# Kernel optimization log

Measured on AMD Instinct MI355X. Metric: run time of the kernel, lower is better.

## Reference

```python
import jax, jax.numpy as jnp
import numpy as np
from jax import lax

STATE_LEN = 5
N_BASE = 4
N_STATES = N_BASE ** STATE_LEN      # 1024
ALPHA_LEN = N_BASE + 1              # 5 (blank + 4 bases)
BLANK_SCORE = 2.0
SCALE = 5.0
NEG = -1e30                         # log-zero surrogate (avoids -inf NaNs)

def _make_idx():
    s = np.arange(N_STATES)
    stay = s[:, None]
    # torch: arange(1024).repeat_interleave(4).reshape(4,-1).T -> idx[j,1+b] = b*256 + j//4
    move = np.repeat(s, N_BASE).reshape(N_BASE, -1).T
    return jnp.asarray(np.concatenate([stay, move], axis=1), dtype=jnp.int32)  # (1024,5)

IDX = _make_idx()

def _logZ_full(scores):
    # full-lattice logZ; scores (T,N,5120)
    T, N, C = scores.shape
    Ms = scores.reshape(T, N, N_STATES, ALPHA_LEN)
    def step(alpha, Mt):
        a = alpha[:, IDX]                          # (N,1024,5) gather of predecessors
        return jax.nn.logsumexp(a + Mt, axis=-1), None
    alpha0 = jnp.zeros((N, N_STATES), scores.dtype)
    alphaT, _ = lax.scan(step, alpha0, Ms)
    return jax.nn.logsumexp(alphaT, axis=-1)       # (N,)

def _prepare_ctc_scores(scores, targets):
    # scores (T,N,C), targets (N,Lmax) base ids in 1..4
    t = jnp.clip(targets - 1, 0)
    T, N, C = scores.shape
    Lmax = t.shape[1]
    n = Lmax - (STATE_LEN - 1)
    stay_idx = sum(t[:, i:n + i] * (N_BASE ** (STATE_LEN - i - 1)) for i in range(STATE_LEN)) * ALPHA_LEN
    move_idx = stay_idx[:, 1:] + t[:, :n - 1] + 1
    stay = jnp.take_along_axis(scores, jnp.broadcast_to(stay_idx[None], (T, N, n)), axis=2)
    move = jnp.take_along_axis(scores, jnp.broadcast_to(move_idx[None], (T, N, n - 1)), axis=2)
    return stay, move

def _ctc_logZ(stay, move, lens):
    # stay (T,N,L), move (T,N,L-1), lens (N,) effective kmer-path lengths
    T, N, L = stay.shape
    alpha0 = jnp.full((N, L), NEG, stay.dtype).at[:, 0].set(0.0)
    def step(alpha, sm):
        s, m = sm
        moved = jnp.pad(alpha[:, :-1] + m, ((0, 0), (1, 0)), constant_values=NEG)
        return jnp.logaddexp(alpha + s, moved), None
    alphaT, _ = lax.scan(step, alpha0, (stay, move))
    return alphaT[jnp.arange(N), lens - 1]

def setup_inputs() -> dict:
    key = jax.random.key(0)
    k1, k2, k3, k4, k5, k6 = jax.random.split(key, 6)
    B, T, D, Lmax = 16, 512, 512, 256
    hs_pad = jax.random.normal(k1, (B, T, D), dtype=jnp.float32)
    hlens = jnp.full((B,), T, dtype=jnp.int32)
    ys_pad = jax.random.randint(k2, (B, Lmax), 1, 5, dtype=jnp.int32)
    ys_lens = jax.random.randint(k3, (B,), 64, Lmax + 1, dtype=jnp.int32)
    W = jax.random.normal(k4, (4096, D), dtype=jnp.float32) * 0.02
    b = jax.random.normal(k5, (4096,), dtype=jnp.float32) * 0.01
    return {"hs_pad": hs_pad, "hlens": hlens, "ys_pad": ys_pad, "ys_lens": ys_lens, "W": W, "b": b}

def reference(hs_pad, hlens, ys_pad, ys_lens, W, b):
    x = jnp.transpose(hs_pad, (1, 0, 2))                 # (T,B,D)
    scores = jnp.tanh(x @ W.T + b) * SCALE               # (T,N,4096)
    T, N, C = scores.shape
    scores = jnp.pad(scores.reshape(T, N, C // N_BASE, N_BASE),
                     ((0, 0), (0, 0), (0, 0), (1, 0)), constant_values=BLANK_SCORE)
    scores = scores.reshape(T, N, -1).astype(jnp.float32)  # (T,N,5120)
    # normalise: subtract full-lattice logZ / T
    logZ = _logZ_full(scores)
    norm = scores - logZ[:, None] / T                    # (N,1) broadcasts over (T,N,C)
    stay, move = _prepare_ctc_scores(norm, ys_pad)
    logz = _ctc_logZ(stay, move, ys_lens + 1 - STATE_LEN)
    loss = -(logz / ys_lens.astype(scores.dtype))        # (N,) (reduction=None in forward)
    scores_bt = jnp.transpose(scores, (1, 0, 2))
    return loss, scores_bt, scores_bt
```

## Files before the change

### kernel.cpp

```cpp
#include <hip/hip_runtime.h>
#include <hip/hip_bf16.h>
#include <hip/hip_fp16.h>
#include <math.h>

#define T_STEPS 512
#define NB      16
#define D_IN    512
#define CG      4096
#define CO      5120
#define LMAX    252
#define NEGF    (-1e30f)
#define SCORES_SZ 41943040LL
#define L2E 1.4426950408889634f
#define LN2 0.6931471805599453f
#define STAYT 0.36787944117144233f

typedef __attribute__((ext_vector_type(8))) short bf16x8;
typedef __attribute__((ext_vector_type(4))) float f32x4;

__device__ __forceinline__ float tanh5(float x) {
    x = fminf(fmaxf(x, -15.f), 15.f);
    float e = __expf(2.f * x);
    return 5.f * (e - 1.f) / (e + 1.f);
}
__device__ __forceinline__ unsigned short f2bf(float v) {
    __hip_bfloat16 h = __float2bfloat16(v);
    return *reinterpret_cast<unsigned short*>(&h);
}
__device__ __forceinline__ float h2f(unsigned short s) {
    union { unsigned short u; _Float16 h; } c; c.u = s;
    return (float)c.h;
}
__device__ __forceinline__ unsigned short f2h(float v) {
    union { unsigned short u; _Float16 h; } c; c.h = (_Float16)v;
    return c.u;
}
__device__ __forceinline__ void cvt8(uint4 u, float* g) {
    g[0] = h2f((unsigned short)(u.x & 0xffff)); g[1] = h2f((unsigned short)(u.x >> 16));
    g[2] = h2f((unsigned short)(u.y & 0xffff)); g[3] = h2f((unsigned short)(u.y >> 16));
    g[4] = h2f((unsigned short)(u.z & 0xffff)); g[5] = h2f((unsigned short)(u.z >> 16));
    g[6] = h2f((unsigned short)(u.w & 0xffff)); g[7] = h2f((unsigned short)(u.w >> 16));
}
__device__ __forceinline__ void xbar() {
    __builtin_amdgcn_sched_barrier(0);
    asm volatile("s_waitcnt lgkmcnt(0)");
    __builtin_amdgcn_s_barrier();
    __builtin_amdgcn_sched_barrier(0);
}
__device__ __forceinline__ void gll16(const unsigned short* g, unsigned short* l) {
    __builtin_amdgcn_global_load_lds((const __attribute__((address_space(1))) void*)g,
                                     (__attribute__((address_space(3))) void*)l, 16, 0, 0);
}

__global__ __launch_bounds__(256) void cvt_bf16_kernel(const float* __restrict__ src,
                                                       unsigned short* __restrict__ dst,
                                                       int n4) {
    int i = blockIdx.x * 256 + threadIdx.x;
    if (i < n4) {
        float4 v = *(reinterpret_cast<const float4*>(src) + i);
        ushort4 o;
        o.x = f2bf(v.x); o.y = f2bf(v.y); o.z = f2bf(v.z); o.w = f2bf(v.w);
        *(reinterpret_cast<ushort4*>(dst) + i) = o;
    }
}

template <bool WSE>
__global__ __launch_bounds__(256) void crf_gemm_bf16(
    const unsigned short* __restrict__ A16,
    const unsigned short* __restrict__ W16,
    const float* __restrict__ bias,
    float* __restrict__ out,
    unsigned short* __restrict__ e16)
{
    __shared__ unsigned short As[128 * 64];
    __shared__ unsigned short Bs[128 * 64];
    const int tid  = threadIdx.x;
    const int lane = tid & 63;
    const int wv   = __builtin_amdgcn_readfirstlane(tid >> 6);
    const int wr   = wv >> 1, wc = wv & 1;
    const int m0   = blockIdx.y * 128;
    const int n0   = blockIdx.x * 128;
    const int wbase = tid & 192;

    f32x4 acc[4][4];
    #pragma unroll
    for (int i = 0; i < 4; ++i)
        #pragma unroll
        for (int j = 0; j < 4; ++j) acc[i][j] = (f32x4){0.f, 0.f, 0.f, 0.f};

    const int l15 = lane & 15, lj = lane >> 4, l7 = lane & 7;

    for (int k0 = 0; k0 < D_IN; k0 += 64) {
        __syncthreads();
        #pragma unroll
        for (int i = 0; i < 4; ++i) {
            const int c   = i * 256 + tid;
            const int row = c >> 3;
            const int jg  = (c & 7) ^ (row & 7);
            const unsigned short* ga = A16 + (size_t)(m0 + row) * D_IN + k0 + jg * 8;
            const unsigned short* gb = W16 + (size_t)(n0 + row) * D_IN + k0 + jg * 8;
            gll16(ga, As + (size_t)(i * 256 + wbase) * 8);
            gll16(gb, Bs + (size_t)(i * 256 + wbase) * 8);
        }
        __syncthreads();
        #pragma unroll
        for (int ks = 0; ks < 2; ++ks) {
            bf16x8 af[4], bb[4];
            #pragma unroll
            for (int mi = 0; mi < 4; ++mi) {
                const int row = wr * 64 + mi * 16 + l15;
                const int jsw = (ks * 4 + lj) ^ l7;
                af[mi] = *reinterpret_cast<const bf16x8*>(&As[row * 64 + jsw * 8]);
            }
            #pragma unroll
            for (int ni = 0; ni < 4; ++ni) {
                const int row = wc * 64 + ni * 16 + l15;
                const int jsw = (ks * 4 + lj) ^ l7;
                bb[ni] = *reinterpret_cast<const bf16x8*>(&Bs[row * 64 + jsw * 8]);
            }
            #pragma unroll
            for (int mi = 0; mi < 4; ++mi)
                #pragma unroll
                for (int ni = 0; ni < 4; ++ni)
                    acc[mi][ni] = __builtin_amdgcn_mfma_f32_16x16x32_bf16(
                        af[mi], bb[ni], acc[mi][ni], 0, 0, 0);
        }
    }

    float bv[4];
    #pragma unroll
    for (int ni = 0; ni < 4; ++ni) bv[ni] = bias[n0 + wc * 64 + ni * 16 + l15];

    #pragma unroll
    for (int mi = 0; mi < 4; ++mi) {
        #pragma unroll
        for (int r = 0; r < 4; ++r) {
            const int m = m0 + wr * 64 + mi * 16 + lj * 4 + r;
            float* r1 = out + 16 + (size_t)m * CO;
            #pragma unroll
            for (int ni = 0; ni < 4; ++ni) {
                const int n = n0 + wc * 64 + ni * 16 + l15;
                const float v = tanh5(acc[mi][ni][r] + bv[ni]);
                const int ch = (n >> 2) * 5 + (n & 3) + 1;
                r1[ch] = v;
                r1[ch + SCORES_SZ] = v;
                if ((l15 & 3) == 0) {
                    r1[ch - 1] = 2.0f;
                    r1[ch - 1 + SCORES_SZ] = 2.0f;
                }
                if (WSE) e16[(size_t)m * CG + n] = f2h(__expf(v - 3.0f));
            }
        }
    }
}

__global__ __launch_bounds__(256) void fb2_kernel(
    const unsigned short* __restrict__ e16,
    const int* __restrict__ ys_pad,
    const int* __restrict__ ys_lens,
    float* __restrict__ FA, float* __restrict__ FAe,
    float* __restrict__ FB, float* __restrict__ FBe,
    float* __restrict__ CAL, float* __restrict__ CBE)
{
    __shared__ float buf[2][1024];
    __shared__ float wmax4[4];
    __shared__ int tcl[256];
    const int role = blockIdx.x >> 4;
    const int n = blockIdx.x & 15;
    const int q = threadIdx.x;
    const int w = q >> 6, lane = q & 63;
    if (role < 2) {
        const bool FWD = (role == 0);
        const unsigned short* eb = e16 + (size_t)(n * T_STEPS) * CG + 16 * q;
        float P0 = 1.f, P1 = 1.f, P2 = 1.f, P3 = 1.f, acc = 0.f;
        *(float4*)&buf[0][4 * q] = make_float4(1.f, 1.f, 1.f, 1.f);
        uint4 pf[8][2];
        #pragma unroll
        for (int u = 0; u < 8; ++u) {
            const int row = FWD ? u : (511 - u);
            pf[u][0] = *(const uint4*)(eb + (size_t)row * CG);
            pf[u][1] = *(const uint4*)(eb + (size_t)row * CG + 8);
        }
        xbar();
        int cur = 0;
        for (int t = 0; t < 256; t += 8) {
            #pragma unroll
            for (int u = 0; u < 8; ++u) {
                float g[16];
                cvt8(pf[u][0], g);
                cvt8(pf[u][1], g + 8);
                int tn = t + u + 8; if (tn > 255) tn = 255;
                const int row = FWD ? tn : (511 - tn);
                pf[u][0] = *(const uint4*)(eb + (size_t)row * CG);
                pf[u][1] = *(const uint4*)(eb + (size_t)row * CG + 8);
                float n0, n1, n2, n3;
                if (FWD) {
                    const float b0 = buf[cur][q];
                    const float b1 = buf[cur][q + 256];
                    const float b2 = buf[cur][q + 512];
                    const float b3 = buf[cur][q + 768];
                    n0 = fmaf(STAYT, P0, fmaf(g[0],  b0, g[1]  * b1) + fmaf(g[2],  b2, g[3]  * b3));
                    n1 = fmaf(STAYT, P1, fmaf(g[4],  b0, g[5]  * b1) + fmaf(g[6],  b2, g[7]  * b3));
                    n2 = fmaf(STAYT, P2, fmaf(g[8],  b0, g[9]  * b1) + fmaf(g[10], b2, g[11] * b3));
                    n3 = fmaf(STAYT, P3, fmaf(g[12], b0, g[13] * b1) + fmaf(g[14], b2, g[15] * b3));
                } else {
                    const float4 b4 = *(const float4*)&buf[cur][4 * q];
                    n0 = fmaf(STAYT, P0, fmaf(g[0], b4.x, g[4] * b4.y) + fmaf(g[8],  b4.z, g[12] * b4.w));
                    n1 = fmaf(STAYT, P1, fmaf(g[1], b4.x, g[5] * b4.y) + fmaf(g[9],  b4.z, g[13] * b4.w));
                    n2 = fmaf(STAYT, P2, fmaf(g[2], b4.x, g[6] * b4.y) + fmaf(g[10], b4.z, g[14] * b4.w));
                    n3 = fmaf(STAYT, P3, fmaf(g[3], b4.x, g[7] * b4.y) + fmaf(g[11], b4.z, g[15] * b4.w));
                }
                if (((t + u) & 7) == 1) {
                    const float wm = fmaxf(fmaxf(wmax4[0], wmax4[1]), fmaxf(wmax4[2], wmax4[3]));
                    const int e = (int)((__float_as_uint(wm) >> 23) & 0xff) - 127;
                    const float c = __uint_as_float((unsigned)(127 - e) << 23);
                    n0 *= c; n1 *= c; n2 *= c; n3 *= c;
                    acc += (float)e;
                }
                P0 = n0; P1 = n1; P2 = n2; P3 = n3;
                if (FWD) {
                    *(float4*)&buf[cur ^ 1][4 * q] = make_float4(P0, P1, P2, P3);
                } else {
                    buf[cur ^ 1][q]       = P0;
                    buf[cur ^ 1][q + 256] = P1;
                    buf[cur ^ 1][q + 512] = P2;
                    buf[cur ^ 1][q + 768] = P3;
                }
                if (((t + u) & 7) == 0) {
                    float m = fmaxf(fmaxf(P0, P1), fmaxf(P2, P3));
                    #pragma unroll
                    for (int msk = 1; msk < 64; msk <<= 1)
                        m = fmaxf(m, __shfl_xor(m, msk, 64));
                    if (lane == 0) wmax4[w] = m;
                }
                xbar();
                cur ^= 1;
            }
        }
        if (FWD) {
            *(float4*)&FA[n * 1024 + 4 * q] = make_float4(P0, P1, P2, P3);
            if (q == 0) FAe[n] = acc;
        } else {
            FB[n * 1024 + q]       = P0;
            FB[n * 1024 + q + 256] = P1;
            FB[n * 1024 + q + 512] = P2;
            FB[n * 1024 + q + 768] = P3;
            if (q == 0) FBe[n] = acc;
        }
    } else {
        float* abuf = &buf[0][0];
        const bool FWD = (role == 2);
        tcl[q] = max(ys_pad[n * 256 + q] - 1, 0);
        xbar();
        int mch = 0; bool val;
        if (FWD) {
            val = (q >= 1 && q < LMAX);
            if (val) {
                const int code = tcl[q] * 256 + tcl[q + 1] * 64 + tcl[q + 2] * 16
                               + tcl[q + 3] * 4 + tcl[q + 4];
                mch = code * 4 + tcl[q - 1];
            }
        } else {
            val = (q < LMAX - 1);
            if (val) {
                const int code = tcl[q + 1] * 256 + tcl[q + 2] * 64 + tcl[q + 3] * 16
                               + tcl[q + 4] * 4 + tcl[q + 5];
                mch = code * 4 + tcl[q];
            }
        }
        const int li = ys_lens[n] - 5;
        float a = FWD ? ((q == 0) ? 0.f : NEGF)
                      : ((q == li) ? 0.f : NEGF);
        abuf[q] = a;
        const unsigned short* eb = e16 + (size_t)(n * T_STEPS) * CG + mch;
        unsigned short pv[16];
        #pragma unroll
        for (int s = 0; s < 16; ++s) {
            const int row = FWD ? s : (511 - s);
            pv[s] = eb[(size_t)row * CG];
        }
        xbar();
        const float STAY2 = (2.0f - 3.0f) * L2E;
        int cur = 0;
        for (int t = 0; t < 256; t += 16) {
            #pragma unroll
            for (int u = 0; u < 16; ++u) {
                const float g2 = val ? __builtin_amdgcn_logf(h2f(pv[u])) : NEGF;
                int tn = t + u + 16; if (tn > 255) tn = 255;
                const int row = FWD ? tn : (511 - tn);
                pv[u] = eb[(size_t)row * CG];
                float nb;
                if (FWD) nb = (q > 0)   ? abuf[cur * 256 + q - 1] : NEGF;
                else     nb = (q < 255) ? abuf[cur * 256 + q + 1] : NEGF;
                const float st = a + STAY2;
                const float mv = nb + g2;
                const float mx = fmaxf(st, mv);
                const float mn = fminf(st, mv);
                a = mx + __builtin_amdgcn_logf(1.f + __builtin_amdgcn_exp2f(mn - mx));
                abuf[(cur ^ 1) * 256 + q] = a;
                xbar();
                cur ^= 1;
            }
        }
        if (FWD) CAL[n * 256 + q] = a;
        else     CBE[n * 256 + q] = a;
    }
}

__global__ __launch_bounds__(256) void combine2_kernel(
    const float* __restrict__ FA, const float* __restrict__ FAe,
    const float* __restrict__ FB, const float* __restrict__ FBe,
    const float* __restrict__ CAL, const float* __restrict__ CBE,
    const int* __restrict__ ys_lens,
    float* __restrict__ out)
{
    __shared__ float red[256];
    __shared__ float lz;
    const int n = blockIdx.x;
    const int q = threadIdx.x;
    float s = 0.f;
    #pragma unroll
    for (int k = 0; k < 4; ++k)
        s += FA[n * 1024 + 4 * q + k] * FB[n * 1024 + 4 * q + k];
    red[q] = s; __syncthreads();
    for (int off = 128; off > 0; off >>= 1) {
        if (q < off) red[q] += red[q + off];
        __syncthreads();
    }
    if (q == 0) lz = FAe[n] + FBe[n] + __builtin_amdgcn_logf(red[0]);
    __syncthreads();
    const float x = CAL[n * 256 + q] + CBE[n * 256 + q];
    red[q] = x; __syncthreads();
    for (int off = 128; off > 0; off >>= 1) {
        if (q < off) red[q] = fmaxf(red[q], red[q + off]);
        __syncthreads();
    }
    const float m = red[0]; __syncthreads();
    red[q] = __builtin_amdgcn_exp2f(x - m); __syncthreads();
    for (int off = 128; off > 0; off >>= 1) {
        if (q < off) red[q] += red[q + off];
        __syncthreads();
    }
    if (q == 0) {
        const float un = m + __builtin_amdgcn_logf(red[0]);
        out[n] = -(LN2 * (un - lz) / (float)ys_lens[n]);
    }
}

__global__ __launch_bounds__(1024) void crf_fwd_kernel(
    const float* __restrict__ scores,
    const int* __restrict__ ys_pad,
    const int* __restrict__ ys_lens,
    float* __restrict__ ws)
{
    const int blk = blockIdx.x;
    const float STAY = 2.0f * L2E;
    if (blk < NB) {
        const int n = blk;
        const int s = threadIdx.x;
        __shared__ float buf[2][1024];
        __shared__ float red[1024];
        float alpha = 0.f;
        buf[0][s] = 0.f;
        const int j0 = s >> 2;
        const float* rowp = scores + (size_t)(n * T_STEPS) * CO + 5 * s + 1;
        float pm[4][4];
        #pragma unroll
        for (int u = 0; u < 4; ++u) {
            const float* r = rowp + (size_t)u * CO;
            pm[u][0] = r[0]; pm[u][1] = r[1]; pm[u][2] = r[2]; pm[u][3] = r[3];
        }
        __syncthreads();
        int cur = 0;
        for (int t = 0; t < T_STEPS; t += 4) {
            #pragma unroll
            for (int u = 0; u < 4; ++u) {
                const float m1 = pm[u][0], m2 = pm[u][1], m3 = pm[u][2], m4 = pm[u][3];
                int tp = t + u + 4; if (tp > T_STEPS - 1) tp = T_STEPS - 1;
                const float* r = rowp + (size_t)tp * CO;
                pm[u][0] = r[0]; pm[u][1] = r[1]; pm[u][2] = r[2]; pm[u][3] = r[3];
                const float b1 = buf[cur][j0];
                const float b2 = buf[cur][j0 + 256];
                const float b3 = buf[cur][j0 + 512];
                const float b4 = buf[cur][j0 + 768];
                const float a0 = alpha + STAY;
                const float a1 = fmaf(m1, L2E, b1);
                const float a2 = fmaf(m2, L2E, b2);
                const float a3 = fmaf(m3, L2E, b3);
                const float a4 = fmaf(m4, L2E, b4);
                const float mx = fmaxf(fmaxf(fmaxf(a0, a1), fmaxf(a2, a3)), a4);
                const float sum = __builtin_amdgcn_exp2f(a0 - mx) + __builtin_amdgcn_exp2f(a1 - mx)
                                + __builtin_amdgcn_exp2f(a2 - mx) + __builtin_amdgcn_exp2f(a3 - mx)
                                + __builtin_amdgcn_exp2f(a4 - mx);
                alpha = mx + __builtin_amdgcn_logf(sum);
                buf[cur ^ 1][s] = alpha;
                __syncthreads();
                cur ^= 1;
            }
        }
        red[s] = alpha;
        __syncthreads();
        for (int off = 512; off > 0; off >>= 1) {
            if (s < off) red[s] = fmaxf(red[s], red[s + off]);
            __syncthreads();
        }
        const float gmax = red[0];
        __syncthreads();
        red[s] = __builtin_amdgcn_exp2f(alpha - gmax);
        __syncthreads();
        for (int off = 512; off > 0; off >>= 1) {
            if (s < off) red[s] += red[s + off];
            __syncthreads();
        }
        if (s == 0) ws[n] = LN2 * (gmax + __builtin_amdgcn_logf(red[0]));
    } else {
        const int n = blk - NB;
        const int i = threadIdx.x;
        __shared__ float abuf[2][LMAX];
        __shared__ int tcl[256];
        if (i < 256) tcl[i] = max(ys_pad[n * 256 + i] - 1, 0);
        __syncthreads();
        int mch = -1;
        if (i >= 1 && i < LMAX) {
            const int code = tcl[i] * 256 + tcl[i + 1] * 64 + tcl[i + 2] * 16
                           + tcl[i + 3] * 4 + tcl[i + 4];
            mch = code * 5 + tcl[i - 1] + 1;
        }
        float alpha = (i == 0) ? 0.f : NEGF;
        if (i < LMAX) abuf[0][i] = alpha;
        const float* base = scores + (size_t)(n * T_STEPS) * CO;
        const size_t moff = (mch >= 0) ? (size_t)mch : 0;
        float pg[4];
        #pragma unroll
        for (int u = 0; u < 4; ++u) pg[u] = base[(size_t)u * CO + moff];
        __syncthreads();
        int cur = 0;
        for (int t = 0; t < T_STEPS; t += 4) {
            #pragma unroll
            for (int u = 0; u < 4; ++u) {
                const float g = pg[u];
                int tp = t + u + 4; if (tp > T_STEPS - 1) tp = T_STEPS - 1;
                pg[u] = base[(size_t)tp * CO + moff];
                if (i < LMAX) {
                    const float a_stay = alpha + STAY;
                    const float prev = (i > 0) ? abuf[cur][i - 1] : NEGF;
                    const float a_mv = (i > 0) ? fmaf(g, L2E, prev) : NEGF;
                    const float mx = fmaxf(a_stay, a_mv);
                    const float mn = fminf(a_stay, a_mv);
                    alpha = mx + __builtin_amdgcn_logf(1.f + __builtin_amdgcn_exp2f(mn - mx));
                    abuf[cur ^ 1][i] = alpha;
                }
                __syncthreads();
                cur ^= 1;
            }
        }
        if (i == ys_lens[n] - 5) ws[NB + n] = alpha * LN2;
    }
}

__global__ void crf_loss_kernel(const float* __restrict__ ws,
                                const int* __restrict__ ys_lens,
                                float* __restrict__ out)
{
    const int n = threadIdx.x;
    if (n < NB) {
        const float logz = ws[NB + n] - ws[n];
        out[n] = -(logz / (float)ys_lens[n]);
    }
}

extern "C" void kernel_launch(void* const* d_in, const int* in_sizes, int n_in,
                              void* d_out, int out_size, void* d_ws, size_t ws_size,
                              hipStream_t stream)
{
    const float* hs      = (const float*)d_in[0];
    const int*   ys_pad  = (const int*)d_in[2];
    const int*   ys_lens = (const int*)d_in[3];
    const float* W       = (const float*)d_in[4];
    const float* bias    = (const float*)d_in[5];
    float* out = (float*)d_out;
    float* ws  = (float*)d_ws;

    const size_t A_ELEMS = (size_t)8192 * 512;
    const size_t W_ELEMS = (size_t)4096 * 512;
    const size_t E_ELEMS = (size_t)8192 * 4096;
    const size_t X_FLOATS = (size_t)16 * 1024 * 2 + 32 + (size_t)16 * 256 * 2;
    const size_t NEED = 256 + (A_ELEMS + W_ELEMS + E_ELEMS) * 2 + X_FLOATS * 4;

    unsigned short* A16 = (unsigned short*)((char*)d_ws + 256);
    unsigned short* W16 = A16 + A_ELEMS;
    unsigned short* E16 = W16 + W_ELEMS;
    float* FA  = (float*)(E16 + E_ELEMS);
    float* FAe = FA + 16 * 1024;
    float* FB  = FAe + 16;
    float* FBe = FB + 16 * 1024;
    float* CAL = FBe + 16;
    float* CBE = CAL + 16 * 256;

    cvt_bf16_kernel<<<(int)(A_ELEMS / 4 / 256), 256, 0, stream>>>(hs, A16, (int)(A_ELEMS / 4));
    cvt_bf16_kernel<<<(int)(W_ELEMS / 4 / 256), 256, 0, stream>>>(W, W16, (int)(W_ELEMS / 4));
    dim3 grid(CG / 128, (NB * T_STEPS) / 128);

    if (ws_size >= NEED) {
        crf_gemm_bf16<true><<<grid, 256, 0, stream>>>(A16, W16, bias, out, E16);
        fb2_kernel<<<64, 256, 0, stream>>>(E16, ys_pad, ys_lens, FA, FAe, FB, FBe, CAL, CBE);
        combine2_kernel<<<16, 256, 0, stream>>>(FA, FAe, FB, FBe, CAL, CBE, ys_lens, out);
    } else {
        crf_gemm_bf16<false><<<grid, 256, 0, stream>>>(A16, W16, bias, out, nullptr);
        crf_fwd_kernel<<<2 * NB, 1024, 0, stream>>>(out + 16, ys_pad, ys_lens, ws);
        crf_loss_kernel<<<1, 64, 0, stream>>>(ws, ys_lens, out);
    }
}
```

Before: 214.0 us.

## Fuse two CRF steps per barrier and run CTC recursion in one wavefront

The full-lattice forward/backward now advances two time steps per block barrier. Each thread recomputes the intermediate alpha values it needs from a shared-memory copy of the neighbouring transition scores, which halves the number of barriers at the cost of redundant arithmetic and more LDS traffic. The CTC path recursion now runs in a single 64-lane wavefront with four states per lane, using cross-lane shuffles instead of LDS plus a block barrier every step. Padded LDS indexing is added to reduce bank conflicts.

Measured after the change: 273.9 us. +28.0%, slower.

```diff
diff --git a/kernel.cpp b/kernel.cpp
--- a/kernel.cpp
+++ b/kernel.cpp
@@ -41,15 +41,14 @@
     g[4] = h2f((unsigned short)(u.z & 0xffff)); g[5] = h2f((unsigned short)(u.z >> 16));
     g[6] = h2f((unsigned short)(u.w & 0xffff)); g[7] = h2f((unsigned short)(u.w >> 16));
 }
-__device__ __forceinline__ void xbar() {
-    __builtin_amdgcn_sched_barrier(0);
-    asm volatile("s_waitcnt lgkmcnt(0)");
-    __builtin_amdgcn_s_barrier();
-    __builtin_amdgcn_sched_barrier(0);
-}
 __device__ __forceinline__ void gll16(const unsigned short* g, unsigned short* l) {
     __builtin_amdgcn_global_load_lds((const __attribute__((address_space(1))) void*)g,
                                      (__attribute__((address_space(3))) void*)l, 16, 0, 0);
+}
+__device__ __forceinline__ int sk(int j) { return j + (j >> 5); }
+__device__ __forceinline__ float laddexp2(float x, float y) {
+    const float mx = fmaxf(x, y), mn = fminf(x, y);
+    return mx + __builtin_amdgcn_logf(1.f + __builtin_amdgcn_exp2f(mn - mx));
 }
 
 __global__ __launch_bounds__(256) void cvt_bf16_kernel(const float* __restrict__ src,
@@ -154,7 +153,7 @@
     }
 }
 
-__global__ __launch_bounds__(256) void fb2_kernel(
+__global__ __launch_bounds__(256) void fb6_kernel(
     const unsigned short* __restrict__ e16,
     const int* __restrict__ ys_pad,
     const int* __restrict__ ys_lens,
@@ -162,83 +161,166 @@
     float* __restrict__ FB, float* __restrict__ FBe,
     float* __restrict__ CAL, float* __restrict__ CBE)
 {
-    __shared__ float buf[2][1024];
-    __shared__ float wmax4[4];
-    __shared__ int tcl[256];
+    __shared__ uint4 SH4[1681];
     const int role = blockIdx.x >> 4;
     const int n = blockIdx.x & 15;
     const int q = threadIdx.x;
     const int w = q >> 6, lane = q & 63;
+    const unsigned short* eb = e16 + (size_t)(n * T_STEPS) * CG;
+
     if (role < 2) {
+        uint4* st0 = SH4;
+        uint4* st1 = SH4 + 576;
+        float* ab0 = (float*)(SH4 + 1152);
+        float* ab1 = ab0 + 1056;
+        float* wmax4 = (float*)(SH4 + 1680);
         const bool FWD = (role == 0);
-        const unsigned short* eb = e16 + (size_t)(n * T_STEPS) * CG + 16 * q;
+        const unsigned short* ebq = eb + 16 * q;
+        const int stIdx = 2 * q + (q >> 3);
+
         float P0 = 1.f, P1 = 1.f, P2 = 1.f, P3 = 1.f, acc = 0.f;
-        *(float4*)&buf[0][4 * q] = make_float4(1.f, 1.f, 1.f, 1.f);
-        uint4 pf[8][2];
-        #pragma unroll
-        for (int u = 0; u < 8; ++u) {
-            const int row = FWD ? u : (511 - u);
-            pf[u][0] = *(const uint4*)(eb + (size_t)row * CG);
-            pf[u][1] = *(const uint4*)(eb + (size_t)row * CG + 8);
-        }
-        xbar();
+        *(float4*)&ab0[4 * q + (q >> 3)] = make_float4(1.f, 1.f, 1.f, 1.f);
+
+        uint4 pfA[4][2], pfB[4][2];
+        #pragma unroll
+        for (int j = 0; j < 4; ++j) {
+            const int r0 = FWD ? (2 * j)     : (511 - 2 * j);
+            const int r1 = FWD ? (2 * j + 1) : (510 - 2 * j);
+            pfA[j][0] = *(const uint4*)(ebq + (size_t)r0 * CG);
+            pfA[j][1] = *(const uint4*)(ebq + (size_t)r0 * CG + 8);
+            pfB[j][0] = *(const uint4*)(ebq + (size_t)r1 * CG);
+            pfB[j][1] = *(const uint4*)(ebq + (size_t)r1 * CG + 8);
+        }
+        st0[stIdx] = pfA[0][0]; st0[stIdx + 1] = pfA[0][1];
+        __syncthreads();
+
         int cur = 0;
-        for (int t = 0; t < 256; t += 8) {
-            #pragma unroll
-            for (int u = 0; u < 8; ++u) {
-                float g[16];
-                cvt8(pf[u][0], g);
-                cvt8(pf[u][1], g + 8);
-                int tn = t + u + 8; if (tn > 255) tn = 255;
-                const int row = FWD ? tn : (511 - tn);
-                pf[u][0] = *(const uint4*)(eb + (size_t)row * CG);
-                pf[u][1] = *(const uint4*)(eb + (size_t)row * CG + 8);
-                float n0, n1, n2, n3;
+        const int h = __builtin_amdgcn_readfirstlane(q >> 6);
+        for (int t4 = 0; t4 < 128; t4 += 4) {
+            #pragma unroll
+            for (int u = 0; u < 4; ++u) {
+                const int i = t4 + u;
+                const uint4 oAa = pfA[u][0], oAb = pfA[u][1];
+                const uint4 oBa = pfB[u][0], oBb = pfB[u][1];
+                {
+                    int rn0, rn1;
+                    if (FWD) { rn0 = 2 * (i + 4); if (rn0 > 255) rn0 = 255; rn1 = rn0 < 255 ? rn0 + 1 : 255; }
+                    else     { rn0 = 511 - 2 * (i + 4); if (rn0 < 256) rn0 = 256; rn1 = rn0 > 256 ? rn0 - 1 : 256; }
+                    pfA[u][0] = *(const uint4*)(ebq + (size_t)rn0 * CG);
+                    pfA[u][1] = *(const uint4*)(ebq + (size_t)rn0 * CG + 8);
+                    pfB[u][0] = *(const uint4*)(ebq + (size_t)rn1 * CG);
+                    pfB[u][1] = *(const uint4*)(ebq + (size_t)rn1 * CG + 8);
+                }
+                float gA[16], gB[16];
+                cvt8(oAa, gA); cvt8(oAb, gA + 8);
+                cvt8(oBa, gB); cvt8(oBb, gB + 8);
+                const float* abR = (cur == 0) ? ab0 : ab1;
+                float* abW = (cur == 0) ? ab1 : ab0;
+                const uint4* stR = ((i & 1) == 0) ? st0 : st1;
+                uint4* stW = ((i & 1) == 0) ? st1 : st0;
+                float o0, o1, o2, o3;
                 if (FWD) {
-                    const float b0 = buf[cur][q];
-                    const float b1 = buf[cur][q + 256];
-                    const float b2 = buf[cur][q + 512];
-                    const float b3 = buf[cur][q + 768];
-                    n0 = fmaf(STAYT, P0, fmaf(g[0],  b0, g[1]  * b1) + fmaf(g[2],  b2, g[3]  * b3));
-                    n1 = fmaf(STAYT, P1, fmaf(g[4],  b0, g[5]  * b1) + fmaf(g[6],  b2, g[7]  * b3));
-                    n2 = fmaf(STAYT, P2, fmaf(g[8],  b0, g[9]  * b1) + fmaf(g[10], b2, g[11] * b3));
-                    n3 = fmaf(STAYT, P3, fmaf(g[12], b0, g[13] * b1) + fmaf(g[14], b2, g[15] * b3));
+                    const float A0a = abR[sk(q)];
+                    const float A1a = abR[sk(q + 256)];
+                    const float A2a = abR[sk(q + 512)];
+                    const float A3a = abR[sk(q + 768)];
+                    float I0 = fmaf(STAYT, P0, fmaf(gA[0],  A0a, gA[1]  * A1a) + fmaf(gA[2],  A2a, gA[3]  * A3a));
+                    float I1 = fmaf(STAYT, P1, fmaf(gA[4],  A0a, gA[5]  * A1a) + fmaf(gA[6],  A2a, gA[7]  * A3a));
+                    float I2 = fmaf(STAYT, P2, fmaf(gA[8],  A0a, gA[9]  * A1a) + fmaf(gA[10], A2a, gA[11] * A3a));
+                    float I3 = fmaf(STAYT, P3, fmaf(gA[12], A0a, gA[13] * A1a) + fmaf(gA[14], A2a, gA[15] * A3a));
+                    float Im[4];
+                    const int jb = q >> 2;
+                    const int o  = (4 * q) & 15;
+                    const int hi8 = o >> 3;
+                    const bool sel = (o & 4) != 0;
+                    #pragma unroll
+                    for (int m = 0; m < 4; ++m) {
+                        const int qc = jb + 64 * m;
+                        const uint4 sv = stR[2 * qc + (qc >> 3) + hi8];
+                        const unsigned int w0 = sel ? sv.z : sv.x;
+                        const unsigned int w1 = sel ? sv.w : sv.y;
+                        const float c0 = abR[sk(jb + 64 * m)];
+                        const float c1 = abR[sk(jb + 64 * m + 256)];
+                        const float c2 = abR[sk(jb + 64 * m + 512)];
+                        const float c3 = abR[sk(jb + 64 * m + 768)];
+                        const float Amv = (m == 0) ? A0a : (m == 1) ? A1a : (m == 2) ? A2a : A3a;
+                        Im[m] = fmaf(STAYT, Amv,
+                                 fmaf(h2f((unsigned short)(w0 & 0xffff)), c0,
+                                      h2f((unsigned short)(w0 >> 16)) * c1)
+                               + fmaf(h2f((unsigned short)(w1 & 0xffff)), c2,
+                                      h2f((unsigned short)(w1 >> 16)) * c3));
+                    }
+                    o0 = fmaf(STAYT, I0, fmaf(gB[0],  Im[0], gB[1]  * Im[1]) + fmaf(gB[2],  Im[2], gB[3]  * Im[3]));
+                    o1 = fmaf(STAYT, I1, fmaf(gB[4],  Im[0], gB[5]  * Im[1]) + fmaf(gB[6],  Im[2], gB[7]  * Im[3]));
+                    o2 = fmaf(STAYT, I2, fmaf(gB[8],  Im[0], gB[9]  * Im[1]) + fmaf(gB[10], Im[2], gB[11] * Im[3]));
+                    o3 = fmaf(STAYT, I3, fmaf(gB[12], Im[0], gB[13] * Im[1]) + fmaf(gB[14], Im[2], gB[15] * Im[3]));
                 } else {
-                    const float4 b4 = *(const float4*)&buf[cur][4 * q];
-                    n0 = fmaf(STAYT, P0, fmaf(g[0], b4.x, g[4] * b4.y) + fmaf(g[8],  b4.z, g[12] * b4.w));
-                    n1 = fmaf(STAYT, P1, fmaf(g[1], b4.x, g[5] * b4.y) + fmaf(g[9],  b4.z, g[13] * b4.w));
-                    n2 = fmaf(STAYT, P2, fmaf(g[2], b4.x, g[6] * b4.y) + fmaf(g[10], b4.z, g[14] * b4.w));
-                    n3 = fmaf(STAYT, P3, fmaf(g[3], b4.x, g[7] * b4.y) + fmaf(g[11], b4.z, g[15] * b4.w));
-                }
-                if (((t + u) & 7) == 1) {
+                    const float4 D = *(const float4*)&abR[4 * q + (q >> 3)];
+                    float Jm0 = fmaf(STAYT, P0, fmaf(gA[0], D.x, gA[4] * D.y) + fmaf(gA[8],  D.z, gA[12] * D.w));
+                    float Jm1 = fmaf(STAYT, P1, fmaf(gA[1], D.x, gA[5] * D.y) + fmaf(gA[9],  D.z, gA[13] * D.w));
+                    float Jm2 = fmaf(STAYT, P2, fmaf(gA[2], D.x, gA[6] * D.y) + fmaf(gA[10], D.z, gA[14] * D.w));
+                    float Jm3 = fmaf(STAYT, P3, fmaf(gA[3], D.x, gA[7] * D.y) + fmaf(gA[11], D.z, gA[15] * D.w));
+                    float Jd[4];
+                    const float Dd[4] = {D.x, D.y, D.z, D.w};
+                    #pragma unroll
+                    for (int d = 0; d < 4; ++d) {
+                        const int r = (4 * q + d) & 255;
+                        const float4 S = *(const float4*)&abR[4 * r + (r >> 3)];
+                        const int idx = 2 * r + (r >> 3);
+                        const uint4 sa = stR[idx];
+                        const uint4 sb = stR[idx + 1];
+                        const unsigned int wa0 = (h & 2) ? sa.y : sa.x;
+                        const unsigned int wa1 = (h & 2) ? sa.w : sa.z;
+                        const unsigned int wb0 = (h & 2) ? sb.y : sb.x;
+                        const unsigned int wb1 = (h & 2) ? sb.w : sb.z;
+                        const float e0 = h2f((unsigned short)((h & 1) ? (wa0 >> 16) : (wa0 & 0xffff)));
+                        const float e1 = h2f((unsigned short)((h & 1) ? (wa1 >> 16) : (wa1 & 0xffff)));
+                        const float e2 = h2f((unsigned short)((h & 1) ? (wb0 >> 16) : (wb0 & 0xffff)));
+                        const float e3 = h2f((unsigned short)((h & 1) ? (wb1 >> 16) : (wb1 & 0xffff)));
+                        Jd[d] = fmaf(STAYT, Dd[d], fmaf(e0, S.x, e1 * S.y) + fmaf(e2, S.z, e3 * S.w));
+                    }
+                    o0 = fmaf(STAYT, Jm0, fmaf(gB[0], Jd[0], gB[4] * Jd[1]) + fmaf(gB[8],  Jd[2], gB[12] * Jd[3]));
+                    o1 = fmaf(STAYT, Jm1, fmaf(gB[1], Jd[0], gB[5] * Jd[1]) + fmaf(gB[9],  Jd[2], gB[13] * Jd[3]));
+                    o2 = fmaf(STAYT, Jm2, fmaf(gB[2], Jd[0], gB[6] * Jd[1]) + fmaf(gB[10], Jd[2], gB[14] * Jd[3]));
+                    o3 = fmaf(STAYT, Jm3, fmaf(gB[3], Jd[0], gB[7] * Jd[1]) + fmaf(gB[11], Jd[2], gB[15] * Jd[3]));
+                }
+                if ((i & 3) == 1) {
                     const float wm = fmaxf(fmaxf(wmax4[0], wmax4[1]), fmaxf(wmax4[2], wmax4[3]));
                     const int e = (int)((__float_as_uint(wm) >> 23) & 0xff) - 127;
                     const float c = __uint_as_float((unsigned)(127 - e) << 23);
-                    n0 *= c; n1 *= c; n2 *= c; n3 *= c;
+                    o0 *= c; o1 *= c; o2 *= c; o3 *= c;
                     acc += (float)e;
                 }
-                P0 = n0; P1 = n1; P2 = n2; P3 = n3;
+                P0 = o0; P1 = o1; P2 = o2; P3 = o3;
                 if (FWD) {
-                    *(float4*)&buf[cur ^ 1][4 * q] = make_float4(P0, P1, P2, P3);
+                    *(float4*)&abW[4 * q + (q >> 3)] = make_float4(P0, P1, P2, P3);
                 } else {
-                    buf[cur ^ 1][q]       = P0;
-                    buf[cur ^ 1][q + 256] = P1;
-                    buf[cur ^ 1][q + 512] = P2;
-                    buf[cur ^ 1][q + 768] = P3;
-                }
-                if (((t + u) & 7) == 0) {
+                    abW[sk(q)]       = P0;
+                    abW[sk(q + 256)] = P1;
+                    abW[sk(q + 512)] = P2;
+                    abW[sk(q + 768)] = P3;
+                }
+                if ((i & 3) == 0) {
                     float m = fmaxf(fmaxf(P0, P1), fmaxf(P2, P3));
                     #pragma unroll
                     for (int msk = 1; msk < 64; msk <<= 1)
                         m = fmaxf(m, __shfl_xor(m, msk, 64));
                     if (lane == 0) wmax4[w] = m;
                 }
-                xbar();
+                if (i < 127) {
+                    const uint4 s0 = pfA[(u + 1) & 3][0];
+                    const uint4 s1 = pfA[(u + 1) & 3][1];
+                    stW[stIdx] = s0; stW[stIdx + 1] = s1;
+                }
+                __syncthreads();
                 cur ^= 1;
             }
         }
         if (FWD) {
-            *(float4*)&FA[n * 1024 + 4 * q] = make_float4(P0, P1, P2, P3);
+            FA[n * 1024 + 4 * q + 0] = P0;
+            FA[n * 1024 + 4 * q + 1] = P1;
+            FA[n * 1024 + 4 * q + 2] = P2;
+            FA[n * 1024 + 4 * q + 3] = P3;
             if (q == 0) FAe[n] = acc;
         } else {
             FB[n * 1024 + q]       = P0;
@@ -248,62 +330,85 @@
             if (q == 0) FBe[n] = acc;
         }
     } else {
-        float* abuf = &buf[0][0];
+        int* tcl = (int*)SH4;
+        tcl[q] = max(ys_pad[n * 256 + q] - 1, 0);
+        __syncthreads();
+        if (q >= 64) return;
         const bool FWD = (role == 2);
-        tcl[q] = max(ys_pad[n * 256 + q] - 1, 0);
-        xbar();
-        int mch = 0; bool val;
+        const int L = q;
+        int mch[4]; bool val[4];
+        #pragma unroll
+        for (int d = 0; d < 4; ++d) {
+            const int p = 4 * L + d;
+            if (FWD) {
+                val[d] = (p >= 1 && p < LMAX);
+                if (val[d]) {
+                    const int code = tcl[p] * 256 + tcl[p + 1] * 64 + tcl[p + 2] * 16
+                                   + tcl[p + 3] * 4 + tcl[p + 4];
+                    mch[d] = code * 4 + tcl[p - 1];
+                } else mch[d] = 0;
+            } else {
+                val[d] = (p < LMAX - 1);
+                if (val[d]) {
+                    const int code = tcl[p + 1] * 256 + tcl[p + 2] * 64 + tcl[p + 3] * 16
+                                   + tcl[p + 4] * 4 + tcl[p + 5];
+                    mch[d] = code * 4 + tcl[p];
+                } else mch[d] = 0;
+            }
+        }
+        const int li = ys_lens[n] - 5;
+        float a0, a1, a2, a3;
         if (FWD) {
-            val = (q >= 1 && q < LMAX);
-            if (val) {
-                const int code = tcl[q] * 256 + tcl[q + 1] * 64 + tcl[q + 2] * 16
-                               + tcl[q + 3] * 4 + tcl[q + 4];
-                mch = code * 4 + tcl[q - 1];
-            }
+            a0 = (4 * L == 0) ? 0.f : NEGF; a1 = NEGF; a2 = NEGF; a3 = NEGF;
         } else {
-            val = (q < LMAX - 1);
-            if (val) {
-                const int code = tcl[q + 1] * 256 + tcl[q + 2] * 64 + tcl[q + 3] * 16
-                               + tcl[q + 4] * 4 + tcl[q + 5];
-                mch = code * 4 + tcl[q];
-            }
-        }
-        const int li = ys_lens[n] - 5;
-        float a = FWD ? ((q == 0) ? 0.f : NEGF)
-                      : ((q == li) ? 0.f : NEGF);
-        abuf[q] = a;
-        const unsigned short* eb = e16 + (size_t)(n * T_STEPS) * CG + mch;
-        unsigned short pv[16];
-        #pragma unroll
-        for (int s = 0; s < 16; ++s) {
+            a0 = (4 * L + 0 == li) ? 0.f : NEGF;
+            a1 = (4 * L + 1 == li) ? 0.f : NEGF;
+            a2 = (4 * L + 2 == li) ? 0.f : NEGF;
+            a3 = (4 * L + 3 == li) ? 0.f : NEGF;
+        }
+        unsigned short pv[8][4];
+        #pragma unroll
+        for (int s = 0; s < 8; ++s) {
             const int row = FWD ? s : (511 - s);
-            pv[s] = eb[(size_t)row * CG];
-        }
-        xbar();
-        const float STAY2 = (2.0f - 3.0f) * L2E;
-        int cur = 0;
-        for (int t = 0; t < 256; t += 16) {
-            #pragma unroll
-            for (int u = 0; u < 16; ++u) {
-                const float g2 = val ? __builtin_amdgcn_logf(h2f(pv[u])) : NEGF;
-                int tn = t + u + 16; if (tn > 255) tn = 255;
+            #pragma unroll
+            for (int d = 0; d < 4; ++d) pv[s][d] = eb[(size_t)row * CG + mch[d]];
+        }
+        const float ST2 = (2.0f - 3.0f) * L2E;
+        for (int t = 0; t < 256; t += 8) {
+            #pragma unroll
+            for (int u = 0; u < 8; ++u) {
+                float g0 = val[0] ? __builtin_amdgcn_logf(h2f(pv[u][0])) : NEGF;
+                float g1 = val[1] ? __builtin_amdgcn_logf(h2f(pv[u][1])) : NEGF;
+                float g2 = val[2] ? __builtin_amdgcn_logf(h2f(pv[u][2])) : NEGF;
+                float g3 = val[3] ? __builtin_amdgcn_logf(h2f(pv[u][3])) : NEGF;
+                int tn = t + u + 8; if (tn > 255) tn = 255;
                 const int row = FWD ? tn : (511 - tn);
-                pv[u] = eb[(size_t)row * CG];
-                float nb;
-                if (FWD) nb = (q > 0)   ? abuf[cur * 256 + q - 1] : NEGF;
-                else     nb = (q < 255) ? abuf[cur * 256 + q + 1] : NEGF;
-                const float st = a + STAY2;
-                const float mv = nb + g2;
-                const float mx = fmaxf(st, mv);
-                const float mn = fminf(st, mv);
-                a = mx + __builtin_amdgcn_logf(1.f + __builtin_amdgcn_exp2f(mn - mx));
-                abuf[(cur ^ 1) * 256 + q] = a;
-                xbar();
-                cur ^= 1;
-            }
-        }
-        if (FWD) CAL[n * 256 + q] = a;
-        else     CBE[n * 256 + q] = a;
+                #pragma unroll
+                for (int d = 0; d < 4; ++d) pv[u][d] = eb[(size_t)row * CG + mch[d]];
+                float n0, n1, n2, n3;
+                if (FWD) {
+                    float pA = __shfl_up(a3, 1, 64);
+                    if (L == 0) pA = NEGF;
+                    n0 = laddexp2(a0 + ST2, pA + g0);
+                    n1 = laddexp2(a1 + ST2, a0 + g1);
+                    n2 = laddexp2(a2 + ST2, a1 + g2);
+                    n3 = laddexp2(a3 + ST2, a2 + g3);
+                } else {
+                    float nP = __shfl_down(a0, 1, 64);
+                    if (L == 63) nP = NEGF;
+                    n3 = laddexp2(a3 + ST2, nP + g3);
+                    n2 = laddexp2(a2 + ST2, a3 + g2);
+                    n1 = laddexp2(a1 + ST2, a2 + g1);
+                    n0 = laddexp2(a0 + ST2, a1 + g0);
+                }
+                a0 = n0; a1 = n1; a2 = n2; a3 = n3;
+            }
+        }
+        float* dst = FWD ? CAL : CBE;
+        dst[n * 256 + 4 * L + 0] = a0;
+        dst[n * 256 + 4 * L + 1] = a1;
+        dst[n * 256 + 4 * L + 2] = a2;
+        dst[n * 256 + 4 * L + 3] = a3;
     }
 }
 
@@ -503,7 +608,7 @@
 
     if (ws_size >= NEED) {
         crf_gemm_bf16<true><<<grid, 256, 0, stream>>>(A16, W16, bias, out, E16);
-        fb2_kernel<<<64, 256, 0, stream>>>(E16, ys_pad, ys_lens, FA, FAe, FB, FBe, CAL, CBE);
+        fb6_kernel<<<64, 256, 0, stream>>>(E16, ys_pad, ys_lens, FA, FAe, FB, FBe, CAL, CBE);
         combine2_kernel<<<16, 256, 0, stream>>>(FA, FAe, FB, FBe, CAL, CBE, ys_lens, out);
     } else {
         crf_gemm_bf16<false><<<grid, 256, 0, stream>>>(A16, W16, bias, out, nullptr);
```
